# Performance work log

Measured on AMD Instinct MI355X. Metric: run time of the kernel, lower is better.

Reference implementation:

```python
import jax, jax.numpy as jnp
import numpy as np
import math

N = 100000          # total nodes across all subgraphs
E = 1600000         # directed edges (avg degree 16)
H = 128             # hidden_channels
MAXZ = 1000         # max_z
G = 1000            # number of subgraphs (unique batch ids)
NPG = N // G        # nodes per subgraph
L = 3               # num_layers


def setup_inputs() -> dict:
    key = jax.random.key(0)
    ks = jax.random.split(key, 9)
    z = jax.random.randint(ks[0], (N,), 0, MAXZ, dtype=jnp.int32)
    edge_index = jax.random.randint(ks[1], (2, E), 0, N, dtype=jnp.int32)
    batch = jnp.repeat(jnp.arange(G, dtype=jnp.int32), NPG)  # sorted graph ids
    s = 1.0 / math.sqrt(H)
    z_emb_table = jax.random.normal(ks[2], (MAXZ, H), jnp.float32) * 0.1
    conv_w = jax.random.normal(ks[3], (L, H, H), jnp.float32) * s
    conv_b = jnp.zeros((L, H), jnp.float32)
    mlp_w1 = jax.random.normal(ks[4], (H, H), jnp.float32) * s
    mlp_b1 = jnp.zeros((H,), jnp.float32)
    mlp_w2 = jax.random.normal(ks[5], (H, 1), jnp.float32) * s
    mlp_b2 = jnp.zeros((1,), jnp.float32)
    return {"num_nodes": N, "z": z, "edge_index": edge_index, "batch": batch,
            "z_emb_table": z_emb_table, "conv_w": conv_w, "conv_b": conv_b,
            "mlp_w1": mlp_w1, "mlp_b1": mlp_b1, "mlp_w2": mlp_w2, "mlp_b2": mlp_b2}


def reference(num_nodes, z, edge_index, batch, z_emb_table, conv_w, conv_b,
              mlp_w1, mlp_b1, mlp_w2, mlp_b2):
    # --- GCN normalization (PyG GCNConv: add self-loops, sym deg norm) ---
    loops = jnp.arange(num_nodes, dtype=edge_index.dtype)
    src = jnp.concatenate([edge_index[0], loops])  # [E+N]
    dst = jnp.concatenate([edge_index[1], loops])
    deg = jax.ops.segment_sum(jnp.ones_like(dst, jnp.float32), dst,
                              num_segments=num_nodes)
    dinv = jnp.where(deg > 0, jax.lax.rsqrt(deg), 0.0)
    norm = (dinv[src] * dinv[dst])[:, None]        # [E+N, 1]

    # --- embedding lookup (eval mode: no dropedge/dropout) ---
    x = z_emb_table[z]                             # [N, H]

    # --- stacked GCNConv: linear -> gather -> normalize -> scatter-add ---
    for l in range(L):
        h = x @ conv_w[l]                          # [N, H]
        h = jax.ops.segment_sum(h[src] * norm, dst, num_segments=num_nodes)
        h = h + conv_b[l]
        x = jax.nn.relu(h) if l < L - 1 else h

    # --- center-node pooling: first occurrence of each batch id ---
    first = jnp.concatenate([jnp.array([True]), batch[1:] != batch[:-1]])
    ci = jnp.nonzero(first, size=G)[0]             # [G]
    xs = x[ci] * x[ci + 1]                         # src * dst node features

    # --- MLP head [H, H, 1] (batch_norm=False, eval: dropout off) ---
    h = jax.nn.relu(xs @ mlp_w1 + mlp_b1)
    return h @ mlp_w2 + mlp_b2                     # [G, 1]
```

## Files before the change

kernel.cpp:

```cpp
#include <hip/hip_runtime.h>
#include <hip/hip_fp16.h>

#define HD 128
#define BSH 9
#define NBLKA 256
#define CAP 96
#define EDSCAP 10240
#define CAPB 12288

typedef _Float16 half8_t __attribute__((ext_vector_type(8)));
typedef float floatx4 __attribute__((ext_vector_type(4)));

__device__ inline unsigned pack_h2(float x, float y) {
  __half2 h = __floats2half2_rn(x, y);
  return __builtin_bit_cast(unsigned, h);
}
__device__ inline float2 up_h2(unsigned u) {
  __half2 h = __builtin_bit_cast(__half2, u);
  return __half22float2(h);
}

__device__ inline void add8(float* acc, uint4 r) {
  float2 f;
  f = up_h2(r.x); acc[0] += f.x; acc[1] += f.y;
  f = up_h2(r.y); acc[2] += f.x; acc[3] += f.y;
  f = up_h2(r.z); acc[4] += f.x; acc[5] += f.y;
  f = up_h2(r.w); acc[6] += f.x; acc[7] += f.y;
}

__global__ __launch_bounds__(256) void k_phase0(const int* __restrict__ src,
                                                const int* __restrict__ dst, int E, int nbuck,
                                                unsigned* __restrict__ bpool,
                                                int* __restrict__ counts,
                                                const float* __restrict__ conv_w,
                                                uint4* __restrict__ wfrag,
                                                const int* __restrict__ z,
                                                const float4* __restrict__ emb,
                                                uint2* __restrict__ xh,
                                                const int* __restrict__ batch,
                                                int* __restrict__ ci,
                                                int* __restrict__ flag,
                                                int n, int embBlocks) {
  __shared__ int cnt[512];
  int b = blockIdx.x;
  if (b < NBLKA) {
    for (int i = threadIdx.x; i < nbuck; i += 256) cnt[i] = 0;
    __syncthreads();
    int chunk = (E + NBLKA - 1) / NBLKA;
    int lo = b * chunk, hi = min(E, lo + chunk);
    for (int i = lo + threadIdx.x; i < hi; i += 256) {
      int s = src[i], d = dst[i];
      int bk = d >> BSH;
      int c = atomicAdd(&cnt[bk], 1);
      if (c < CAP)
        bpool[((size_t)bk * NBLKA + b) * CAP + c] =
            ((unsigned)(d & ((1 << BSH) - 1)) << 23) | (unsigned)s;
    }
    __syncthreads();
    for (int bk = threadIdx.x; bk < nbuck; bk += 256) counts[(size_t)bk * NBLKA + b] = cnt[bk];
  } else if (b < NBLKA + 24) {
    int t = (b - NBLKA) * 256 + threadIdx.x;
    int lane = t & 63;
    int s = (t >> 6) & 3;
    int c4 = (t >> 8) & 3;
    int chalf = (t >> 10) & 1;
    int layer = t >> 11;
    int col = chalf * 64 + c4 * 16 + (lane & 15);
    int k0 = s * 32 + (lane >> 4) * 8;
    const float* W = conv_w + (size_t)layer * HD * HD;
    unsigned u[4];
#pragma unroll
    for (int j = 0; j < 4; ++j)
      u[j] = pack_h2(W[(size_t)(k0 + 2 * j) * HD + col], W[(size_t)(k0 + 2 * j + 1) * HD + col]);
    uint4 o; o.x = u[0]; o.y = u[1]; o.z = u[2]; o.w = u[3];
    wfrag[t] = o;
  } else if (b < NBLKA + 24 + embBlocks) {
    int idx = (b - NBLKA - 24) * 256 + threadIdx.x;
    if (idx >= n * 32) return;
    int node = idx >> 5, q = idx & 31;
    float4 v = emb[(size_t)z[node] * 32 + q];
    uint2 o;
    o.x = pack_h2(v.x, v.y);
    o.y = pack_h2(v.z, v.w);
    xh[idx] = o;
  } else {
    int i = (b - NBLKA - 24 - embBlocks) * 256 + threadIdx.x;
    if (i >= n) return;
    flag[i] = 0;
    if (i == 0) flag[n] = 0;
    if (i == 0 || batch[i] != batch[i - 1]) ci[batch[i]] = i;
  }
}

__global__ __launch_bounds__(256) void k_build(const unsigned* __restrict__ bpool,
                                               const int* __restrict__ counts,
                                               int n, float* __restrict__ dinv,
                                               int* __restrict__ rowstart,
                                               int* __restrict__ rowend,
                                               int* __restrict__ col) {
  __shared__ unsigned eds[EDSCAP];
  __shared__ int hist[1 << BSH];
  __shared__ int wsum[256];
  __shared__ int coff[NBLKA + 1];
  int b = blockIdx.x;
  int t = threadIdx.x;
  int v = (t < NBLKA) ? min(counts[(size_t)b * NBLKA + t], CAP) : 0;
  wsum[t] = v;
  __syncthreads();
  for (int off = 1; off < NBLKA; off <<= 1) {
    int x = (t >= off) ? wsum[t - off] : 0;
    __syncthreads();
    wsum[t] += x;
    __syncthreads();
  }
  if (t < NBLKA) coff[t] = wsum[t] - v;
  if (t == NBLKA - 1) coff[NBLKA] = wsum[NBLKA - 1];
  __syncthreads();
  int total = min(coff[NBLKA], EDSCAP);
  int w = t >> 6, lane = t & 63;
  for (int blk = w; blk < NBLKA; blk += 4) {
    int off0 = coff[blk], len = coff[blk + 1] - off0;
    const unsigned* seg = bpool + ((size_t)b * NBLKA + blk) * CAP;
    for (int i = lane; i < len; i += 64)
      if (off0 + i < EDSCAP) eds[off0 + i] = seg[i];
  }
  for (int i = t; i < (1 << BSH); i += 256) hist[i] = 0;
  __syncthreads();
  for (int i = t; i < total; i += 256) atomicAdd(&hist[eds[i] >> 23], 1);
  __syncthreads();
  int base = b << BSH;
  int nn = min(1 << BSH, n - base);
  int a0 = hist[2 * t], a1 = hist[2 * t + 1];
  int s = a0 + a1;
  wsum[t] = s;
  __syncthreads();
  for (int off = 1; off < 256; off <<= 1) {
    int x = (t >= off) ? wsum[t - off] : 0;
    __syncthreads();
    wsum[t] += x;
    __syncthreads();
  }
  int excl = wsum[t] - s;
  int cbase = b * CAPB;
  if (2 * t < nn) {
    rowstart[base + 2 * t] = cbase + excl;
    rowend[base + 2 * t] = cbase + excl + a0;
    dinv[base + 2 * t] = 1.0f / sqrtf((float)(a0 + 1));
  }
  if (2 * t + 1 < nn) {
    rowstart[base + 2 * t + 1] = cbase + excl + a0;
    rowend[base + 2 * t + 1] = cbase + excl + s;
    dinv[base + 2 * t + 1] = 1.0f / sqrtf((float)(a1 + 1));
  }
  hist[2 * t] = cbase + excl;
  hist[2 * t + 1] = cbase + excl + a0;
  __syncthreads();
  for (int i = t; i < total; i += 256) {
    unsigned pk = eds[i];
    int dl = pk >> 23;
    int pos = atomicAdd(&hist[dl], 1);
    col[pos] = (int)(pk & 0x7FFFFF);
  }
}

__global__ __launch_bounds__(64) void k_active(const int* __restrict__ ci,
                                               const int* __restrict__ rowstart,
                                               const int* __restrict__ rowend,
                                               const int* __restrict__ col,
                                               int g2, int* __restrict__ flag,
                                               int* __restrict__ list, int n) {
  int lane = threadIdx.x;
  int vid = blockIdx.x * 64 + lane;
  bool haveRow = vid < g2;
  int* nactive = flag + n;
  int node = 0, e = 0, end = 0;
  if (haveRow) {
    node = ci[vid >> 1] + (vid & 1);
    e = rowstart[node];
    end = rowend[node];
  }
  bool neu = haveRow && (atomicExch(&flag[node], 1) == 0);
  unsigned long long m = __ballot(neu);
  int base = 0;
  if (lane == 0 && m) base = atomicAdd(nactive, __popcll(m));
  base = __shfl(base, 0);
  if (neu) list[base + __popcll(m & ((1ULL << lane) - 1))] = node;
  for (;;) {
    bool act = haveRow && (e < end);
    if (!__any(act)) break;
    int s = act ? col[e] : 0;
    bool nw = act && (atomicExch(&flag[s], 1) == 0);
    unsigned long long mm = __ballot(nw);
    int b2 = 0;
    if (lane == 0 && mm) b2 = atomicAdd(nactive, __popcll(mm));
    b2 = __shfl(b2, 0);
    if (nw) list[b2 + __popcll(mm & ((1ULL << lane) - 1))] = s;
    ++e;
  }
}

__global__ __launch_bounds__(256) void k_gemm_mfma(const uint4* __restrict__ Xh,
                                                   const uint4* __restrict__ wfrag,
                                                   const float* __restrict__ dinv,
                                                   uint2* __restrict__ Yh,
                                                   int n, int nwaves) {
  int lane = threadIdx.x & 63;
  int gw = blockIdx.x * 4 + (threadIdx.x >> 6);
  int chalf = gw & 1;
  int nrb = (n + 15) >> 4;
  int h = lane >> 4;

  half8_t wf[16];
#pragma unroll
  for (int i = 0; i < 16; ++i) {
    uint4 t = wfrag[((chalf * 4 + (i >> 2)) * 4 + (i & 3)) * 64 + lane];
    wf[i] = __builtin_bit_cast(half8_t, t);
  }

  for (int rb = gw >> 1; rb < nrb; rb += (nwaves >> 1)) {
    int row0 = rb * 16;
    int xr = row0 + (lane & 15);
    if (xr > n - 1) xr = n - 1;
    const uint4* xrow = Xh + (size_t)xr * 16;
    half8_t bf[4];
#pragma unroll
    for (int s = 0; s < 4; ++s)
      bf[s] = __builtin_bit_cast(half8_t, xrow[s * 4 + h]);
    floatx4 acc[4];
#pragma unroll
    for (int c4 = 0; c4 < 4; ++c4) acc[c4] = (floatx4){0.f, 0.f, 0.f, 0.f};
#pragma unroll
    for (int s = 0; s < 4; ++s) {
#pragma unroll
      for (int c4 = 0; c4 < 4; ++c4)
        acc[c4] = __builtin_amdgcn_mfma_f32_16x16x32_f16(wf[c4 * 4 + s], bf[s], acc[c4], 0, 0, 0);
    }
    int orow = row0 + (lane & 15);
    float dv = dinv[xr];
    if (orow < n) {
#pragma unroll
      for (int c4 = 0; c4 < 4; ++c4) {
        int colbase = chalf * 64 + c4 * 16 + h * 4;
        uint2 o;
        o.x = pack_h2(acc[c4][0] * dv, acc[c4][1] * dv);
        o.y = pack_h2(acc[c4][2] * dv, acc[c4][3] * dv);
        Yh[(size_t)orow * 32 + (colbase >> 2)] = o;
      }
    }
  }
}

__global__ __launch_bounds__(256) void k_gemmL(const uint4* __restrict__ Xh,
                                               const uint4* __restrict__ wfrag,
                                               const float* __restrict__ dinv,
                                               uint2* __restrict__ Yh,
                                               const int* __restrict__ list,
                                               const int* __restrict__ nactive,
                                               int nwaves) {
  int na = *nactive;
  int lane = threadIdx.x & 63;
  int gw = blockIdx.x * 4 + (threadIdx.x >> 6);
  int chalf = gw & 1;
  int nrb = (na + 15) >> 4;
  int h = lane >> 4;

  half8_t wf[16];
#pragma unroll
  for (int i = 0; i < 16; ++i) {
    uint4 t = wfrag[((chalf * 4 + (i >> 2)) * 4 + (i & 3)) * 64 + lane];
    wf[i] = __builtin_bit_cast(half8_t, t);
  }

  for (int rb = gw >> 1; rb < nrb; rb += (nwaves >> 1)) {
    int i = rb * 16 + (lane & 15);
    int xr = list[i < na ? i : na - 1];
    const uint4* xrow = Xh + (size_t)xr * 16;
    half8_t bf[4];
#pragma unroll
    for (int s = 0; s < 4; ++s)
      bf[s] = __builtin_bit_cast(half8_t, xrow[s * 4 + h]);
    floatx4 acc[4];
#pragma unroll
    for (int c4 = 0; c4 < 4; ++c4) acc[c4] = (floatx4){0.f, 0.f, 0.f, 0.f};
#pragma unroll
    for (int s = 0; s < 4; ++s) {
#pragma unroll
      for (int c4 = 0; c4 < 4; ++c4)
        acc[c4] = __builtin_amdgcn_mfma_f32_16x16x32_f16(wf[c4 * 4 + s], bf[s], acc[c4], 0, 0, 0);
    }
    float dv = dinv[xr];
    if (i < na) {
#pragma unroll
      for (int c4 = 0; c4 < 4; ++c4) {
        int colbase = chalf * 64 + c4 * 16 + h * 4;
        uint2 o;
        o.x = pack_h2(acc[c4][0] * dv, acc[c4][1] * dv);
        o.y = pack_h2(acc[c4][2] * dv, acc[c4][3] * dv);
        Yh[(size_t)xr * 32 + (colbase >> 2)] = o;
      }
    }
  }
}

__global__ __launch_bounds__(256) void k_agg(const uint4* __restrict__ H,
                                             const int* __restrict__ rowstart,
                                             const int* __restrict__ rowend,
                                             const int* __restrict__ col,
                                             const float* __restrict__ dinv,
                                             const float* __restrict__ bias,
                                             uint4* __restrict__ Out, int n, int relu) {
  int li = threadIdx.x & 15;
  int node = blockIdx.x * 16 + (threadIdx.x >> 4);
  if (node >= n) return;
  uint4 srow = H[(size_t)node * 16 + li];
  float acc[8] = {0.f, 0.f, 0.f, 0.f, 0.f, 0.f, 0.f, 0.f};
  add8(acc, srow);
  int e = rowstart[node], end = rowend[node];
  for (; e + 3 < end; e += 4) {
    int c0 = col[e], c1 = col[e + 1], c2 = col[e + 2], c3 = col[e + 3];
    uint4 r0 = H[(size_t)c0 * 16 + li];
    uint4 r1 = H[(size_t)c1 * 16 + li];
    uint4 r2 = H[(size_t)c2 * 16 + li];
    uint4 r3 = H[(size_t)c3 * 16 + li];
    add8(acc, r0);
    add8(acc, r1);
    add8(acc, r2);
    add8(acc, r3);
  }
  for (; e < end; ++e) {
    uint4 r = H[(size_t)col[e] * 16 + li];
    add8(acc, r);
  }
  float dv = dinv[node];
  float4 b0 = ((const float4*)bias)[2 * li];
  float4 b1 = ((const float4*)bias)[2 * li + 1];
  acc[0] = fmaf(dv, acc[0], b0.x); acc[1] = fmaf(dv, acc[1], b0.y);
  acc[2] = fmaf(dv, acc[2], b0.z); acc[3] = fmaf(dv, acc[3], b0.w);
  acc[4] = fmaf(dv, acc[4], b1.x); acc[5] = fmaf(dv, acc[5], b1.y);
  acc[6] = fmaf(dv, acc[6], b1.z); acc[7] = fmaf(dv, acc[7], b1.w);
  if (relu) {
#pragma unroll
    for (int q = 0; q < 8; ++q) acc[q] = fmaxf(acc[q], 0.f);
  }
  uint4 o;
  o.x = pack_h2(acc[0], acc[1]);
  o.y = pack_h2(acc[2], acc[3]);
  o.z = pack_h2(acc[4], acc[5]);
  o.w = pack_h2(acc[6], acc[7]);
  Out[(size_t)node * 16 + li] = o;
}

__global__ __launch_bounds__(256) void k_aggL(const uint4* __restrict__ H,
                                              const int* __restrict__ rowstart,
                                              const int* __restrict__ rowend,
                                              const int* __restrict__ col,
                                              const float* __restrict__ dinv,
                                              const float* __restrict__ bias,
                                              uint4* __restrict__ Out,
                                              const int* __restrict__ list,
                                              const int* __restrict__ nactive) {
  int na = *nactive;
  int li = threadIdx.x & 15;
  int i0 = blockIdx.x * 16 + (threadIdx.x >> 4);
  int stride = gridDim.x * 16;
  for (int i = i0; i < na; i += stride) {
    int node = list[i];
    uint4 srow = H[(size_t)node * 16 + li];
    float acc[8] = {0.f, 0.f, 0.f, 0.f, 0.f, 0.f, 0.f, 0.f};
    add8(acc, srow);
    int e = rowstart[node], end = rowend[node];
    for (; e + 3 < end; e += 4) {
      int c0 = col[e], c1 = col[e + 1], c2 = col[e + 2], c3 = col[e + 3];
      uint4 r0 = H[(size_t)c0 * 16 + li];
      uint4 r1 = H[(size_t)c1 * 16 + li];
      uint4 r2 = H[(size_t)c2 * 16 + li];
      uint4 r3 = H[(size_t)c3 * 16 + li];
      add8(acc, r0);
      add8(acc, r1);
      add8(acc, r2);
      add8(acc, r3);
    }
    for (; e < end; ++e) {
      uint4 r = H[(size_t)col[e] * 16 + li];
      add8(acc, r);
    }
    float dv = dinv[node];
    float4 b0 = ((const float4*)bias)[2 * li];
    float4 b1 = ((const float4*)bias)[2 * li + 1];
    acc[0] = fmaf(dv, acc[0], b0.x); acc[1] = fmaf(dv, acc[1], b0.y);
    acc[2] = fmaf(dv, acc[2], b0.z); acc[3] = fmaf(dv, acc[3], b0.w);
    acc[4] = fmaf(dv, acc[4], b1.x); acc[5] = fmaf(dv, acc[5], b1.y);
    acc[6] = fmaf(dv, acc[6], b1.z); acc[7] = fmaf(dv, acc[7], b1.w);
#pragma unroll
    for (int q = 0; q < 8; ++q) acc[q] = fmaxf(acc[q], 0.f);
    uint4 o;
    o.x = pack_h2(acc[0], acc[1]);
    o.y = pack_h2(acc[2], acc[3]);
    o.z = pack_h2(acc[4], acc[5]);
    o.w = pack_h2(acc[6], acc[7]);
    Out[(size_t)node * 16 + li] = o;
  }
}

__global__ __launch_bounds__(256) void k_aggF(const uint4* __restrict__ H,
                                              const int* __restrict__ rowstart,
                                              const int* __restrict__ rowend,
                                              const int* __restrict__ col,
                                              const float* __restrict__ dinv,
                                              const float* __restrict__ bias,
                                              const int* __restrict__ ci,
                                              uint4* __restrict__ Xc, int g2) {
  int li = threadIdx.x & 15;
  int vid = blockIdx.x * 16 + (threadIdx.x >> 4);
  if (vid >= g2) return;
  int node = ci[vid >> 1] + (vid & 1);
  uint4 srow = H[(size_t)node * 16 + li];
  float acc[8] = {0.f, 0.f, 0.f, 0.f, 0.f, 0.f, 0.f, 0.f};
  add8(acc, srow);
  int e = rowstart[node], end = rowend[node];
  for (; e + 3 < end; e += 4) {
    int c0 = col[e], c1 = col[e + 1], c2 = col[e + 2], c3 = col[e + 3];
    uint4 r0 = H[(size_t)c0 * 16 + li];
    uint4 r1 = H[(size_t)c1 * 16 + li];
    uint4 r2 = H[(size_t)c2 * 16 + li];
    uint4 r3 = H[(size_t)c3 * 16 + li];
    add8(acc, r0);
    add8(acc, r1);
    add8(acc, r2);
    add8(acc, r3);
  }
  for (; e < end; ++e) {
    uint4 r = H[(size_t)col[e] * 16 + li];
    add8(acc, r);
  }
  float dv = dinv[node];
  float4 b0 = ((const float4*)bias)[2 * li];
  float4 b1 = ((const float4*)bias)[2 * li + 1];
  acc[0] = fmaf(dv, acc[0], b0.x); acc[1] = fmaf(dv, acc[1], b0.y);
  acc[2] = fmaf(dv, acc[2], b0.z); acc[3] = fmaf(dv, acc[3], b0.w);
  acc[4] = fmaf(dv, acc[4], b1.x); acc[5] = fmaf(dv, acc[5], b1.y);
  acc[6] = fmaf(dv, acc[6], b1.z); acc[7] = fmaf(dv, acc[7], b1.w);
  uint4 o;
  o.x = pack_h2(acc[0], acc[1]);
  o.y = pack_h2(acc[2], acc[3]);
  o.z = pack_h2(acc[4], acc[5]);
  o.w = pack_h2(acc[6], acc[7]);
  Xc[(size_t)vid * 16 + li] = o;
}

__global__ __launch_bounds__(128) void k_head(const __half* __restrict__ Xc,
                                              const float* __restrict__ W1,
                                              const float* __restrict__ b1,
                                              const float* __restrict__ w2,
                                              const float* __restrict__ b2,
                                              float* __restrict__ out, int G) {
  __shared__ float xs[HD];
  __shared__ float red[HD];
  int g = blockIdx.x;
  int t = threadIdx.x;
  xs[t] = __half2float(Xc[(size_t)(2 * g) * HD + t]) *
          __half2float(Xc[(size_t)(2 * g + 1) * HD + t]);
  __syncthreads();
  float acc = b1[t];
#pragma unroll 8
  for (int k = 0; k < HD; ++k) acc = fmaf(xs[k], W1[k * HD + t], acc);
  acc = fmaxf(acc, 0.f);
  red[t] = acc * w2[t];
  __syncthreads();
  for (int off = 64; off > 0; off >>= 1) {
    if (t < off) red[t] += red[t + off];
    __syncthreads();
  }
  if (t == 0) out[g] = red[0] + b2[0];
}

extern "C" void kernel_launch(void* const* d_in, const int* in_sizes, int n_in,
                              void* d_out, int out_size, void* d_ws, size_t ws_size,
                              hipStream_t stream) {
  (void)n_in; (void)ws_size;
  const int*   z      = (const int*)d_in[1];
  const int*   ei     = (const int*)d_in[2];
  const int*   batch  = (const int*)d_in[3];
  const float* emb    = (const float*)d_in[4];
  const float* conv_w = (const float*)d_in[5];
  const float* conv_b = (const float*)d_in[6];
  const float* w1     = (const float*)d_in[7];
  const float* b1     = (const float*)d_in[8];
  const float* w2     = (const float*)d_in[9];
  const float* b2     = (const float*)d_in[10];
  int n = in_sizes[1];
  int E = in_sizes[2] / 2;
  int G = out_size;
  const int* esrc = ei;
  const int* edst = ei + E;
  int nbuck = (n + (1 << BSH) - 1) >> BSH;

  char* p = (char*)d_ws;
  auto alloc = [&](size_t bytes) { void* r = (void*)p; p += (bytes + 255) / 256 * 256; return r; };
  unsigned* bufA     = (unsigned*)alloc((size_t)n * HD * 2);
  unsigned* bufB     = (unsigned*)alloc((size_t)n * HD * 2);
  unsigned* bufC     = (unsigned*)alloc((size_t)2 * G * HD * 2);
  float*    dinv     = (float*)alloc((size_t)n * 4);
  int*      rowstart = (int*)alloc((size_t)n * 4);
  int*      rowend   = (int*)alloc((size_t)n * 4);
  int*      col      = (int*)alloc((size_t)nbuck * CAPB * 4);
  uint4*    wfrag    = (uint4*)alloc((size_t)3 * 2048 * 16);
  int*      ci       = (int*)alloc((size_t)G * 4);
  int*      flag     = (int*)alloc((size_t)(n + 64) * 4);
  int*      list     = (int*)alloc((size_t)n * 4);
  unsigned* bpool    = (unsigned*)alloc((size_t)nbuck * NBLKA * CAP * 4);
  int*      counts   = (int*)alloc((size_t)nbuck * NBLKA * 4);

  int embBlocks = (n * 32 + 255) / 256;
  int ciBlocks = (n + 255) / 256;
  int g2 = 2 * G;
  int* nactive = flag + n;

  k_phase0<<<NBLKA + 24 + embBlocks + ciBlocks, 256, 0, stream>>>(
      esrc, edst, E, nbuck, bpool, counts, conv_w, wfrag, z, (const float4*)emb,
      (uint2*)bufA, batch, ci, flag, n, embBlocks);
  k_build<<<nbuck, 256, 0, stream>>>(bpool, counts, n, dinv, rowstart, rowend, col);
  k_active<<<(g2 + 63) / 64, 64, 0, stream>>>(ci, rowstart, rowend, col, g2, flag, list, n);

  const int nwaves = 4096;
  k_gemm_mfma<<<nwaves / 4, 256, 0, stream>>>((const uint4*)bufA, wfrag, dinv,
                                              (uint2*)bufB, n, nwaves);
  k_agg<<<(n + 15) / 16, 256, 0, stream>>>((const uint4*)bufB, rowstart, rowend, col, dinv,
                                           conv_b, (uint4*)bufA, n, 1);
  k_gemm_mfma<<<nwaves / 4, 256, 0, stream>>>((const uint4*)bufA, wfrag + 2048, dinv,
                                              (uint2*)bufB, n, nwaves);
  k_aggL<<<1024, 256, 0, stream>>>((const uint4*)bufB, rowstart, rowend, col, dinv,
                                   conv_b + HD, (uint4*)bufA, list, nactive);
  k_gemmL<<<256, 256, 0, stream>>>((const uint4*)bufA, wfrag + 4096, dinv,
                                   (uint2*)bufB, list, nactive, 1024);
  k_aggF<<<(g2 + 15) / 16, 256, 0, stream>>>((const uint4*)bufB, rowstart, rowend, col, dinv,
                                             conv_b + 2 * HD, ci, (uint4*)bufC, g2);

  k_head<<<G, 128, 0, stream>>>((const __half*)bufC, w1, b1, w2, b2, (float*)d_out, G);
}
```

Measured before the change: 239.2 us.

## Fuse embedding, aggregation and next-layer GEMM into single kernels via LDS tiles

Embedding lookup is fused with the first layer's MFMA GEMM, and each aggregation pass is fused with the following layer's GEMM. Each block aggregates 16 rows into a padded shared-memory tile and then runs MFMA on it directly. This removes the round-trip of the intermediate activation matrix through global memory and cuts two to three kernel launches. In exchange every block reloads its weight fragments, and the GEMM now waits behind the irregular gather in the same block, with barriers in between.

```diff
diff --git a/kernel.cpp b/kernel.cpp
--- a/kernel.cpp
+++ b/kernel.cpp
@@ -7,6 +7,7 @@
 #define CAP 96
 #define EDSCAP 10240
 #define CAPB 12288
+#define RPAD 136
 
 typedef _Float16 half8_t __attribute__((ext_vector_type(8)));
 typedef float floatx4 __attribute__((ext_vector_type(4)));
@@ -34,13 +35,10 @@
                                                 int* __restrict__ counts,
                                                 const float* __restrict__ conv_w,
                                                 uint4* __restrict__ wfrag,
-                                                const int* __restrict__ z,
-                                                const float4* __restrict__ emb,
-                                                uint2* __restrict__ xh,
                                                 const int* __restrict__ batch,
                                                 int* __restrict__ ci,
                                                 int* __restrict__ flag,
-                                                int n, int embBlocks) {
+                                                int n) {
   __shared__ int cnt[512];
   int b = blockIdx.x;
   if (b < NBLKA) {
@@ -74,17 +72,8 @@
       u[j] = pack_h2(W[(size_t)(k0 + 2 * j) * HD + col], W[(size_t)(k0 + 2 * j + 1) * HD + col]);
     uint4 o; o.x = u[0]; o.y = u[1]; o.z = u[2]; o.w = u[3];
     wfrag[t] = o;
-  } else if (b < NBLKA + 24 + embBlocks) {
-    int idx = (b - NBLKA - 24) * 256 + threadIdx.x;
-    if (idx >= n * 32) return;
-    int node = idx >> 5, q = idx & 31;
-    float4 v = emb[(size_t)z[node] * 32 + q];
-    uint2 o;
-    o.x = pack_h2(v.x, v.y);
-    o.y = pack_h2(v.z, v.w);
-    xh[idx] = o;
   } else {
-    int i = (b - NBLKA - 24 - embBlocks) * 256 + threadIdx.x;
+    int i = (b - NBLKA - 24) * 256 + threadIdx.x;
     if (i >= n) return;
     flag[i] = 0;
     if (i == 0) flag[n] = 0;
@@ -199,123 +188,86 @@
   }
 }
 
-__global__ __launch_bounds__(256) void k_gemm_mfma(const uint4* __restrict__ Xh,
-                                                   const uint4* __restrict__ wfrag,
-                                                   const float* __restrict__ dinv,
-                                                   uint2* __restrict__ Yh,
-                                                   int n, int nwaves) {
-  int lane = threadIdx.x & 63;
-  int gw = blockIdx.x * 4 + (threadIdx.x >> 6);
-  int chalf = gw & 1;
-  int nrb = (n + 15) >> 4;
-  int h = lane >> 4;
-
-  half8_t wf[16];
-#pragma unroll
-  for (int i = 0; i < 16; ++i) {
-    uint4 t = wfrag[((chalf * 4 + (i >> 2)) * 4 + (i & 3)) * 64 + lane];
-    wf[i] = __builtin_bit_cast(half8_t, t);
-  }
-
-  for (int rb = gw >> 1; rb < nrb; rb += (nwaves >> 1)) {
-    int row0 = rb * 16;
-    int xr = row0 + (lane & 15);
-    if (xr > n - 1) xr = n - 1;
-    const uint4* xrow = Xh + (size_t)xr * 16;
-    half8_t bf[4];
-#pragma unroll
-    for (int s = 0; s < 4; ++s)
-      bf[s] = __builtin_bit_cast(half8_t, xrow[s * 4 + h]);
-    floatx4 acc[4];
-#pragma unroll
-    for (int c4 = 0; c4 < 4; ++c4) acc[c4] = (floatx4){0.f, 0.f, 0.f, 0.f};
+__device__ inline void gemm16(const _Float16* xs, const uint4* __restrict__ wfragL,
+                              const float* __restrict__ dinv, uint2* __restrict__ Yh,
+                              int row0, int nvalid, const int* __restrict__ rowmap,
+                              int tid) {
+  int lane = tid & 63, w = tid >> 6;
+  int chalf = w >> 1, h = lane >> 4;
+  half8_t wf[8];
+#pragma unroll
+  for (int cc = 0; cc < 2; ++cc)
 #pragma unroll
     for (int s = 0; s < 4; ++s) {
-#pragma unroll
-      for (int c4 = 0; c4 < 4; ++c4)
-        acc[c4] = __builtin_amdgcn_mfma_f32_16x16x32_f16(wf[c4 * 4 + s], bf[s], acc[c4], 0, 0, 0);
+      int c4 = 2 * (w & 1) + cc;
+      wf[cc * 4 + s] = __builtin_bit_cast(half8_t,
+          wfragL[((chalf * 4 + c4) * 4 + s) * 64 + lane]);
     }
-    int orow = row0 + (lane & 15);
-    float dv = dinv[xr];
-    if (orow < n) {
-#pragma unroll
-      for (int c4 = 0; c4 < 4; ++c4) {
-        int colbase = chalf * 64 + c4 * 16 + h * 4;
-        uint2 o;
-        o.x = pack_h2(acc[c4][0] * dv, acc[c4][1] * dv);
-        o.y = pack_h2(acc[c4][2] * dv, acc[c4][3] * dv);
-        Yh[(size_t)orow * 32 + (colbase >> 2)] = o;
-      }
+  half8_t bf[4];
+#pragma unroll
+  for (int s = 0; s < 4; ++s)
+    bf[s] = *(const half8_t*)&xs[(size_t)(lane & 15) * RPAD + (s * 4 + h) * 8];
+  floatx4 acc[2];
+  acc[0] = (floatx4){0.f, 0.f, 0.f, 0.f};
+  acc[1] = (floatx4){0.f, 0.f, 0.f, 0.f};
+#pragma unroll
+  for (int s = 0; s < 4; ++s) {
+    acc[0] = __builtin_amdgcn_mfma_f32_16x16x32_f16(wf[s], bf[s], acc[0], 0, 0, 0);
+    acc[1] = __builtin_amdgcn_mfma_f32_16x16x32_f16(wf[4 + s], bf[s], acc[1], 0, 0, 0);
+  }
+  int i = row0 + (lane & 15);
+  if (i < nvalid) {
+    int orow = rowmap ? rowmap[i] : i;
+    float dv = dinv[orow];
+#pragma unroll
+    for (int cc = 0; cc < 2; ++cc) {
+      int c4 = 2 * (w & 1) + cc;
+      int colbase = chalf * 64 + c4 * 16 + h * 4;
+      uint2 o;
+      o.x = pack_h2(acc[cc][0] * dv, acc[cc][1] * dv);
+      o.y = pack_h2(acc[cc][2] * dv, acc[cc][3] * dv);
+      Yh[(size_t)orow * 32 + (colbase >> 2)] = o;
     }
   }
 }
 
-__global__ __launch_bounds__(256) void k_gemmL(const uint4* __restrict__ Xh,
-                                               const uint4* __restrict__ wfrag,
-                                               const float* __restrict__ dinv,
-                                               uint2* __restrict__ Yh,
-                                               const int* __restrict__ list,
-                                               const int* __restrict__ nactive,
-                                               int nwaves) {
-  int na = *nactive;
-  int lane = threadIdx.x & 63;
-  int gw = blockIdx.x * 4 + (threadIdx.x >> 6);
-  int chalf = gw & 1;
-  int nrb = (na + 15) >> 4;
-  int h = lane >> 4;
-
-  half8_t wf[16];
-#pragma unroll
-  for (int i = 0; i < 16; ++i) {
-    uint4 t = wfrag[((chalf * 4 + (i >> 2)) * 4 + (i & 3)) * 64 + lane];
-    wf[i] = __builtin_bit_cast(half8_t, t);
-  }
-
-  for (int rb = gw >> 1; rb < nrb; rb += (nwaves >> 1)) {
-    int i = rb * 16 + (lane & 15);
-    int xr = list[i < na ? i : na - 1];
-    const uint4* xrow = Xh + (size_t)xr * 16;
-    half8_t bf[4];
-#pragma unroll
-    for (int s = 0; s < 4; ++s)
-      bf[s] = __builtin_bit_cast(half8_t, xrow[s * 4 + h]);
-    floatx4 acc[4];
-#pragma unroll
-    for (int c4 = 0; c4 < 4; ++c4) acc[c4] = (floatx4){0.f, 0.f, 0.f, 0.f};
-#pragma unroll
-    for (int s = 0; s < 4; ++s) {
-#pragma unroll
-      for (int c4 = 0; c4 < 4; ++c4)
-        acc[c4] = __builtin_amdgcn_mfma_f32_16x16x32_f16(wf[c4 * 4 + s], bf[s], acc[c4], 0, 0, 0);
-    }
-    float dv = dinv[xr];
-    if (i < na) {
-#pragma unroll
-      for (int c4 = 0; c4 < 4; ++c4) {
-        int colbase = chalf * 64 + c4 * 16 + h * 4;
-        uint2 o;
-        o.x = pack_h2(acc[c4][0] * dv, acc[c4][1] * dv);
-        o.y = pack_h2(acc[c4][2] * dv, acc[c4][3] * dv);
-        Yh[(size_t)xr * 32 + (colbase >> 2)] = o;
-      }
-    }
-  }
-}
-
-__global__ __launch_bounds__(256) void k_agg(const uint4* __restrict__ H,
-                                             const int* __restrict__ rowstart,
-                                             const int* __restrict__ rowend,
-                                             const int* __restrict__ col,
-                                             const float* __restrict__ dinv,
-                                             const float* __restrict__ bias,
-                                             uint4* __restrict__ Out, int n, int relu) {
-  int li = threadIdx.x & 15;
-  int node = blockIdx.x * 16 + (threadIdx.x >> 4);
-  if (node >= n) return;
-  uint4 srow = H[(size_t)node * 16 + li];
+__global__ __launch_bounds__(256) void k_embgemm(const int* __restrict__ z,
+                                                 const float4* __restrict__ emb,
+                                                 const uint4* __restrict__ wfragL,
+                                                 const float* __restrict__ dinv,
+                                                 uint2* __restrict__ Yh, int n) {
+  __shared__ __align__(16) _Float16 xs[16 * RPAD];
+  int tid = threadIdx.x;
+  int grp = tid >> 4, li = tid & 15;
+  int node = blockIdx.x * 16 + grp;
+  int nd = node < n ? node : n - 1;
+  const float4* er = emb + (size_t)z[nd] * 32 + li * 2;
+  float4 f0 = er[0], f1 = er[1];
+  uint4 hx;
+  hx.x = pack_h2(f0.x, f0.y); hx.y = pack_h2(f0.z, f0.w);
+  hx.z = pack_h2(f1.x, f1.y); hx.w = pack_h2(f1.z, f1.w);
+  *(uint4*)&xs[(size_t)grp * RPAD + li * 8] = hx;
+  __syncthreads();
+  gemm16(xs, wfragL, dinv, Yh, blockIdx.x * 16, n, nullptr, tid);
+}
+
+__global__ __launch_bounds__(256) void k_agg_gemm(const uint4* __restrict__ H,
+                                                  const int* __restrict__ rowstart,
+                                                  const int* __restrict__ rowend,
+                                                  const int* __restrict__ col,
+                                                  const float* __restrict__ dinv,
+                                                  const float* __restrict__ bias,
+                                                  const uint4* __restrict__ wfragL,
+                                                  uint2* __restrict__ Yh, int n) {
+  __shared__ __align__(16) _Float16 xs[16 * RPAD];
+  int tid = threadIdx.x;
+  int grp = tid >> 4, li = tid & 15;
+  int node = blockIdx.x * 16 + grp;
+  int nd = node < n ? node : n - 1;
+  uint4 srow = H[(size_t)nd * 16 + li];
   float acc[8] = {0.f, 0.f, 0.f, 0.f, 0.f, 0.f, 0.f, 0.f};
   add8(acc, srow);
-  int e = rowstart[node], end = rowend[node];
+  int e = rowstart[nd], end = rowend[nd];
   for (; e + 3 < end; e += 4) {
     int c0 = col[e], c1 = col[e + 1], c2 = col[e + 2], c3 = col[e + 3];
     uint4 r0 = H[(size_t)c0 * 16 + li];
@@ -331,40 +283,42 @@
     uint4 r = H[(size_t)col[e] * 16 + li];
     add8(acc, r);
   }
-  float dv = dinv[node];
+  float dv = dinv[nd];
   float4 b0 = ((const float4*)bias)[2 * li];
   float4 b1 = ((const float4*)bias)[2 * li + 1];
-  acc[0] = fmaf(dv, acc[0], b0.x); acc[1] = fmaf(dv, acc[1], b0.y);
-  acc[2] = fmaf(dv, acc[2], b0.z); acc[3] = fmaf(dv, acc[3], b0.w);
-  acc[4] = fmaf(dv, acc[4], b1.x); acc[5] = fmaf(dv, acc[5], b1.y);
-  acc[6] = fmaf(dv, acc[6], b1.z); acc[7] = fmaf(dv, acc[7], b1.w);
-  if (relu) {
-#pragma unroll
-    for (int q = 0; q < 8; ++q) acc[q] = fmaxf(acc[q], 0.f);
-  }
-  uint4 o;
-  o.x = pack_h2(acc[0], acc[1]);
-  o.y = pack_h2(acc[2], acc[3]);
-  o.z = pack_h2(acc[4], acc[5]);
-  o.w = pack_h2(acc[6], acc[7]);
-  Out[(size_t)node * 16 + li] = o;
-}
-
-__global__ __launch_bounds__(256) void k_aggL(const uint4* __restrict__ H,
-                                              const int* __restrict__ rowstart,
-                                              const int* __restrict__ rowend,
-                                              const int* __restrict__ col,
-                                              const float* __restrict__ dinv,
-                                              const float* __restrict__ bias,
-                                              uint4* __restrict__ Out,
-                                              const int* __restrict__ list,
-                                              const int* __restrict__ nactive) {
+  acc[0] = fmaxf(fmaf(dv, acc[0], b0.x), 0.f);
+  acc[1] = fmaxf(fmaf(dv, acc[1], b0.y), 0.f);
+  acc[2] = fmaxf(fmaf(dv, acc[2], b0.z), 0.f);
+  acc[3] = fmaxf(fmaf(dv, acc[3], b0.w), 0.f);
+  acc[4] = fmaxf(fmaf(dv, acc[4], b1.x), 0.f);
+  acc[5] = fmaxf(fmaf(dv, acc[5], b1.y), 0.f);
+  acc[6] = fmaxf(fmaf(dv, acc[6], b1.z), 0.f);
+  acc[7] = fmaxf(fmaf(dv, acc[7], b1.w), 0.f);
+  uint4 hx;
+  hx.x = pack_h2(acc[0], acc[1]); hx.y = pack_h2(acc[2], acc[3]);
+  hx.z = pack_h2(acc[4], acc[5]); hx.w = pack_h2(acc[6], acc[7]);
+  *(uint4*)&xs[(size_t)grp * RPAD + li * 8] = hx;
+  __syncthreads();
+  gemm16(xs, wfragL, dinv, Yh, blockIdx.x * 16, n, nullptr, tid);
+}
+
+__global__ __launch_bounds__(256) void k_agg_gemmL(const uint4* __restrict__ H,
+                                                   const int* __restrict__ rowstart,
+                                                   const int* __restrict__ rowend,
+                                                   const int* __restrict__ col,
+                                                   const float* __restrict__ dinv,
+                                                   const float* __restrict__ bias,
+                                                   const uint4* __restrict__ wfragL,
+                                                   uint2* __restrict__ Yh,
+                                                   const int* __restrict__ list,
+                                                   const int* __restrict__ nactive) {
+  __shared__ __align__(16) _Float16 xs[16 * RPAD];
   int na = *nactive;
-  int li = threadIdx.x & 15;
-  int i0 = blockIdx.x * 16 + (threadIdx.x >> 4);
-  int stride = gridDim.x * 16;
-  for (int i = i0; i < na; i += stride) {
-    int node = list[i];
+  int tid = threadIdx.x;
+  int grp = tid >> 4, li = tid & 15;
+  for (int tile = blockIdx.x; tile * 16 < na; tile += gridDim.x) {
+    int i = tile * 16 + grp;
+    int node = list[i < na ? i : na - 1];
     uint4 srow = H[(size_t)node * 16 + li];
     float acc[8] = {0.f, 0.f, 0.f, 0.f, 0.f, 0.f, 0.f, 0.f};
     add8(acc, srow);
@@ -387,18 +341,21 @@
     float dv = dinv[node];
     float4 b0 = ((const float4*)bias)[2 * li];
     float4 b1 = ((const float4*)bias)[2 * li + 1];
-    acc[0] = fmaf(dv, acc[0], b0.x); acc[1] = fmaf(dv, acc[1], b0.y);
-    acc[2] = fmaf(dv, acc[2], b0.z); acc[3] = fmaf(dv, acc[3], b0.w);
-    acc[4] = fmaf(dv, acc[4], b1.x); acc[5] = fmaf(dv, acc[5], b1.y);
-    acc[6] = fmaf(dv, acc[6], b1.z); acc[7] = fmaf(dv, acc[7], b1.w);
-#pragma unroll
-    for (int q = 0; q < 8; ++q) acc[q] = fmaxf(acc[q], 0.f);
-    uint4 o;
-    o.x = pack_h2(acc[0], acc[1]);
-    o.y = pack_h2(acc[2], acc[3]);
-    o.z = pack_h2(acc[4], acc[5]);
-    o.w = pack_h2(acc[6], acc[7]);
-    Out[(size_t)node * 16 + li] = o;
+    acc[0] = fmaxf(fmaf(dv, acc[0], b0.x), 0.f);
+    acc[1] = fmaxf(fmaf(dv, acc[1], b0.y), 0.f);
+    acc[2] = fmaxf(fmaf(dv, acc[2], b0.z), 0.f);
+    acc[3] = fmaxf(fmaf(dv, acc[3], b0.w), 0.f);
+    acc[4] = fmaxf(fmaf(dv, acc[4], b1.x), 0.f);
+    acc[5] = fmaxf(fmaf(dv, acc[5], b1.y), 0.f);
+    acc[6] = fmaxf(fmaf(dv, acc[6], b1.z), 0.f);
+    acc[7] = fmaxf(fmaf(dv, acc[7], b1.w), 0.f);
+    uint4 hx;
+    hx.x = pack_h2(acc[0], acc[1]); hx.y = pack_h2(acc[2], acc[3]);
+    hx.z = pack_h2(acc[4], acc[5]); hx.w = pack_h2(acc[6], acc[7]);
+    *(uint4*)&xs[(size_t)grp * RPAD + li * 8] = hx;
+    __syncthreads();
+    gemm16(xs, wfragL, dinv, Yh, tile * 16, na, list, tid);
+    __syncthreads();
   }
 }
 
@@ -511,30 +468,21 @@
   unsigned* bpool    = (unsigned*)alloc((size_t)nbuck * NBLKA * CAP * 4);
   int*      counts   = (int*)alloc((size_t)nbuck * NBLKA * 4);
 
-  int embBlocks = (n * 32 + 255) / 256;
   int ciBlocks = (n + 255) / 256;
   int g2 = 2 * G;
   int* nactive = flag + n;
 
-  k_phase0<<<NBLKA + 24 + embBlocks + ciBlocks, 256, 0, stream>>>(
-      esrc, edst, E, nbuck, bpool, counts, conv_w, wfrag, z, (const float4*)emb,
-      (uint2*)bufA, batch, ci, flag, n, embBlocks);
+  k_phase0<<<NBLKA + 24 + ciBlocks, 256, 0, stream>>>(
+      esrc, edst, E, nbuck, bpool, counts, conv_w, wfrag, batch, ci, flag, n);
   k_build<<<nbuck, 256, 0, stream>>>(bpool, counts, n, dinv, rowstart, rowend, col);
+  k_embgemm<<<(n + 15) / 16, 256, 0, stream>>>(z, (const float4*)emb, wfrag, dinv,
+                                               (uint2*)bufB, n);
   k_active<<<(g2 + 63) / 64, 64, 0, stream>>>(ci, rowstart, rowend, col, g2, flag, list, n);
-
-  const int nwaves = 4096;
-  k_gemm_mfma<<<nwaves / 4, 256, 0, stream>>>((const uint4*)bufA, wfrag, dinv,
-                                              (uint2*)bufB, n, nwaves);
-  k_agg<<<(n + 15) / 16, 256, 0, stream>>>((const uint4*)bufB, rowstart, rowend, col, dinv,
-                                           conv_b, (uint4*)bufA, n, 1);
-  k_gemm_mfma<<<nwaves / 4, 256, 0, stream>>>((const uint4*)bufA, wfrag + 2048, dinv,
-                                              (uint2*)bufB, n, nwaves);
-  k_aggL<<<1024, 256, 0, stream>>>((const uint4*)bufB, rowstart, rowend, col, dinv,
-                                   conv_b + HD, (uint4*)bufA, list, nactive);
-  k_gemmL<<<256, 256, 0, stream>>>((const uint4*)bufA, wfrag + 4096, dinv,
-                                   (uint2*)bufB, list, nactive, 1024);
+  k_agg_gemm<<<(n + 15) / 16, 256, 0, stream>>>((const uint4*)bufB, rowstart, rowend, col,
+                                                dinv, conv_b, wfrag + 2048, (uint2*)bufA, n);
+  k_agg_gemmL<<<512, 256, 0, stream>>>((const uint4*)bufA, rowstart, rowend, col, dinv,
+                                       conv_b + HD, wfrag + 4096, (uint2*)bufB, list, nactive);
   k_aggF<<<(g2 + 15) / 16, 256, 0, stream>>>((const uint4*)bufB, rowstart, rowend, col, dinv,
                                              conv_b + 2 * HD, ci, (uint4*)bufC, g2);
-
   k_head<<<G, 128, 0, stream>>>((const __half*)bufC, w1, b1, w2, b2, (float*)d_out, G);
 }
```

After: 232.3 us. -2.9%, faster.
